# Optimization experiments

Hardware: AMD Instinct MI355X
Metric: run time of the kernel (lower is better)

Reference implementation:

```python
import jax, jax.numpy as jnp
import numpy as np

B, N, E, H = 2, 4096, 512, 8
D = E // H  # head size


def setup_inputs() -> dict:
    key = jax.random.key(0)
    ks = jax.random.split(key, 11)
    s = 1.0 / np.sqrt(E)
    inp = {
        'q': jax.random.normal(ks[0], (B, N, E), jnp.float32),
        'k': jax.random.normal(ks[1], (B, N, E), jnp.float32),
        'v': jax.random.normal(ks[2], (B, N, E), jnp.float32),
        'Wq': jax.random.uniform(ks[3], (E, E), jnp.float32, -s, s),
        'bq': jax.random.uniform(ks[4], (E,), jnp.float32, -s, s),
        'Wk': jax.random.uniform(ks[5], (E, E), jnp.float32, -s, s),
        'bk': jax.random.uniform(ks[6], (E,), jnp.float32, -s, s),
        'Wv': jax.random.uniform(ks[7], (E, E), jnp.float32, -s, s),
        'bv': jax.random.uniform(ks[8], (E,), jnp.float32, -s, s),
        'Wo': jax.random.uniform(ks[9], (E, E), jnp.float32, -s, s),
        'bo': jax.random.uniform(ks[10], (E,), jnp.float32, -s, s),
    }
    return inp


def reference(q, k, v, Wq, bq, Wk, bk, Wv, bv, Wo, bo):
    # Linear projections (torch Linear: x @ W.T + b)
    qp = (q @ Wq.T + bq).reshape(B, N, H, D).transpose(0, 2, 1, 3)  # [B,H,N,D]
    kp = (k @ Wk.T + bk).reshape(B, N, H, D).transpose(0, 2, 1, 3)
    vp = (v @ Wv.T + bv).reshape(B, N, H, D).transpose(0, 2, 1, 3)
    scores = jnp.einsum('bhnd,bhmd->bhnm', qp, kp) / jnp.sqrt(jnp.float32(D))
    attn = jax.nn.softmax(scores, axis=-1)
    out = jnp.einsum('bhnm,bhmd->bhnd', attn, vp)  # [B,H,N,D]
    out = out.transpose(0, 2, 1, 3).reshape(B, N, E)
    return out @ Wo.T + bo
```

## Files before the change

### kernel.cpp

```cpp
#include <hip/hip_runtime.h>
#include <hip/hip_bf16.h>
#include <cstddef>
#include <cstdint>


typedef __bf16 bf16_t;
typedef __bf16 bf16x8 __attribute__((ext_vector_type(8)));
typedef __bf16 bf16x4 __attribute__((ext_vector_type(4)));
typedef float  f32x4  __attribute__((ext_vector_type(4)));

#define MFMA_BF16 __builtin_amdgcn_mfma_f32_16x16x32_bf16

static __device__ __forceinline__ bf16x8 cvt2(const float4& a, const float4& b) {
  return bf16x8{(bf16_t)a.x,(bf16_t)a.y,(bf16_t)a.z,(bf16_t)a.w,
                (bf16_t)b.x,(bf16_t)b.y,(bf16_t)b.z,(bf16_t)b.w};
}

static __device__ __forceinline__ uint32_t pk2(float a, float b) {
  uint32_t r;
  asm("v_cvt_pk_bf16_f32 %0, %1, %2" : "=v"(r) : "v"(a), "v"(b));
  return r;
}

__global__ void __launch_bounds__(256)
cvt_bf16(const float* __restrict__ q, const float* __restrict__ k,
         const float* __restrict__ v, const float* __restrict__ Wq,
         const float* __restrict__ Wk, const float* __restrict__ Wv,
         const float* __restrict__ Wo,
         bf16_t* __restrict__ qb, bf16_t* __restrict__ kb,
         bf16_t* __restrict__ vb, bf16_t* __restrict__ wq,
         bf16_t* __restrict__ wk, bf16_t* __restrict__ wv,
         bf16_t* __restrict__ wo)
{
  const int CQ = 524288;
  const int CW = 32768;
  const int TOT = 3 * CQ + 4 * CW;
  const int STRIDE = 2048 * 256;
  for (int c = blockIdx.x * 256 + threadIdx.x; c < TOT; c += STRIDE) {
    const float* src; bf16_t* dst; int off;
    if (c < 3 * CQ) {
      const int t = c >> 19;
      const int r = c & (CQ - 1);
      src = (t == 0) ? q : (t == 1) ? k : v;
      dst = (t == 0) ? qb : (t == 1) ? kb : vb;
      off = r << 3;
    } else {
      const int c2 = c - 3 * CQ;
      const int t = c2 >> 15;
      const int r = c2 & (CW - 1);
      src = (t == 0) ? Wq : (t == 1) ? Wk : (t == 2) ? Wv : Wo;
      dst = (t == 0) ? wq : (t == 1) ? wk : (t == 2) ? wv : wo;
      off = r << 3;
    }
    const float4 a = *(const float4*)(src + off);
    const float4 b = *(const float4*)(src + off + 4);
    *(bf16x8*)(dst + off) = cvt2(a, b);
  }
}

__global__ void __launch_bounds__(256, 3)
qkv_proj(const bf16_t* __restrict__ qb, const bf16_t* __restrict__ kb,
         const bf16_t* __restrict__ vb,
         const bf16_t* __restrict__ Wqb, const float* __restrict__ bq,
         const bf16_t* __restrict__ Wkb, const float* __restrict__ bk,
         const bf16_t* __restrict__ Wvb, const float* __restrict__ bv,
         bf16_t* __restrict__ Qp, bf16_t* __restrict__ Kp,
         bf16_t* __restrict__ Vt, float qscale)
{
  __shared__ __align__(16) bf16_t S[2 * 128 * 72];
  bf16_t* As = S;
  bf16_t* Bs = S + 128 * 72;

  const int l     = blockIdx.x;
  const int slice = l >> 8;
  const int inner = l & 255;
  const int mtile = ((inner & 7) << 3) | (inner >> 5);
  const int ntile = (inner >> 3) & 3;
  const int tid   = threadIdx.x;
  const int w     = tid >> 6;
  const int lane  = tid & 63;
  const int lr    = lane & 15;
  const int quad  = lane >> 4;
  const int wm    = w & 1;
  const int wn    = w >> 1;
  const int xrow  = tid >> 1, xcol = (tid & 1) << 5;

  const bf16_t* Xb   = (slice == 0) ? qb  : (slice == 1) ? kb  : vb;
  const bf16_t* W    = (slice == 0) ? Wqb : (slice == 1) ? Wkb : Wvb;
  const float*  bias = (slice == 0) ? bq  : (slice == 1) ? bk  : bv;
  const float scale  = (slice == 0) ? qscale : 1.0f;

  float bvv[4];
#pragma unroll
  for (int ci = 0; ci < 4; ++ci) bvv[ci] = bias[ntile * 128 + wn * 64 + ci * 16 + lr];

  f32x4 acc[4][4] = {};
  bf16x8 xa[4], wa[4];

#pragma unroll
  for (int j = 0; j < 4; ++j) {
    xa[j] = *(const bf16x8*)(Xb + (size_t)(mtile * 128 + xrow) * 512 + xcol + j * 8);
    wa[j] = *(const bf16x8*)(W  + (size_t)(ntile * 128 + xrow) * 512 + xcol + j * 8);
  }
#pragma unroll
  for (int j = 0; j < 4; ++j) {
    *(bf16x8*)(&As[xrow * 72 + xcol + j * 8]) = xa[j];
    *(bf16x8*)(&Bs[xrow * 72 + xcol + j * 8]) = wa[j];
  }
  __syncthreads();

  for (int it = 0; it < 8; ++it) {
    if (it != 7) {
      const int k0 = (it + 1) << 6;
#pragma unroll
      for (int j = 0; j < 4; ++j) {
        xa[j] = *(const bf16x8*)(Xb + (size_t)(mtile * 128 + xrow) * 512 + k0 + xcol + j * 8);
        wa[j] = *(const bf16x8*)(W  + (size_t)(ntile * 128 + xrow) * 512 + k0 + xcol + j * 8);
      }
    }
    bf16x8 af[4][2], bfr[4][2];
#pragma unroll
    for (int mi = 0; mi < 4; ++mi)
#pragma unroll
      for (int kh = 0; kh < 2; ++kh)
        af[mi][kh] = *(const bf16x8*)(&As[(wm * 64 + mi * 16 + lr) * 72 + (kh * 4 + quad) * 8]);
#pragma unroll
    for (int ci = 0; ci < 4; ++ci)
#pragma unroll
      for (int kh = 0; kh < 2; ++kh)
        bfr[ci][kh] = *(const bf16x8*)(&Bs[(wn * 64 + ci * 16 + lr) * 72 + (kh * 4 + quad) * 8]);
#pragma unroll
    for (int mi = 0; mi < 4; ++mi)
#pragma unroll
      for (int ci = 0; ci < 4; ++ci) {
        acc[mi][ci] = MFMA_BF16(af[mi][0], bfr[ci][0], acc[mi][ci], 0, 0, 0);
        acc[mi][ci] = MFMA_BF16(af[mi][1], bfr[ci][1], acc[mi][ci], 0, 0, 0);
      }
    __syncthreads();
    if (it != 7) {
#pragma unroll
      for (int j = 0; j < 4; ++j) {
        *(bf16x8*)(&As[xrow * 72 + xcol + j * 8]) = xa[j];
        *(bf16x8*)(&Bs[xrow * 72 + xcol + j * 8]) = wa[j];
      }
      __syncthreads();
    }
  }

  bf16_t (*Ct)[136] = (bf16_t (*)[136])S;
  if (slice < 2) {
    bf16_t* outQK = (slice == 0) ? Qp : Kp;
#pragma unroll
    for (int mi = 0; mi < 4; ++mi)
#pragma unroll
      for (int ci = 0; ci < 4; ++ci)
#pragma unroll
        for (int r = 0; r < 4; ++r)
          Ct[wm * 64 + mi * 16 + quad * 4 + r][wn * 64 + ci * 16 + lr] =
              (bf16_t)((acc[mi][ci][r] + bvv[ci]) * scale);
    __syncthreads();
    const int r2 = tid >> 1, half = tid & 1;
    const int gm = mtile * 128 + r2;
    const int b = gm >> 12, n = gm & 4095;
    const int gc0 = ntile * 128 + half * 64;
    const int h = gc0 >> 6;
    bf16_t* dst = outQK + (size_t)((b * 8 + h) * 4096 + n) * 64;
#pragma unroll
    for (int j = 0; j < 8; ++j)
      *(bf16x8*)(dst + j * 8) = *(const bf16x8*)(&Ct[r2][half * 64 + j * 8]);
  } else {
#pragma unroll
    for (int mi = 0; mi < 4; ++mi)
#pragma unroll
      for (int ci = 0; ci < 4; ++ci)
#pragma unroll
        for (int r = 0; r < 4; ++r)
          Ct[wn * 64 + ci * 16 + lr][wm * 64 + mi * 16 + quad * 4 + r] =
              (bf16_t)(acc[mi][ci][r] + bvv[ci]);
    __syncthreads();
    const int dline = tid >> 1, half = tid & 1;
    const int gc = ntile * 128 + dline;
    const int h = gc >> 6, dd = gc & 63;
    const int b = (mtile * 128) >> 12;
    const int n0 = (mtile * 128) & 4095;
    bf16_t* dst = Vt + (size_t)((b * 8 + h) * 64 + dd) * 4096 + n0 + half * 64;
#pragma unroll
    for (int j = 0; j < 8; ++j)
      *(bf16x8*)(dst + j * 8) = *(const bf16x8*)(&Ct[dline][half * 64 + j * 8]);
  }
}

__global__ void __launch_bounds__(256, 4)
o_proj(const bf16_t* __restrict__ Xb, const bf16_t* __restrict__ W,
       const float* __restrict__ bias, float* __restrict__ out)
{
  __shared__ __align__(16) bf16_t As[64 * 72];
  __shared__ __align__(16) bf16_t Bs[64 * 72];
  const int l     = blockIdx.x;
  const int mtile = ((l & 7) << 4) | ((l >> 3) & 15);
  const int ntile = l >> 7;
  const int tid   = threadIdx.x;
  const int w     = tid >> 6;
  const int lane  = tid & 63;
  const int lr    = lane & 15;
  const int quad  = lane >> 4;
  const int wm    = w & 1;
  const int wn    = w >> 1;
  const int xrow  = tid >> 2, xcol = (tid & 3) << 4;

  float bvv[2];
#pragma unroll
  for (int ci = 0; ci < 2; ++ci) bvv[ci] = bias[ntile * 64 + wn * 32 + ci * 16 + lr];

  f32x4 acc[2][2] = {};
  bf16x8 xb[2], wb[2];

#pragma unroll
  for (int j = 0; j < 2; ++j) {
    xb[j] = *(const bf16x8*)(Xb + (size_t)(mtile * 64 + xrow) * 512 + xcol + j * 8);
    wb[j] = *(const bf16x8*)(W  + (size_t)(ntile * 64 + xrow) * 512 + xcol + j * 8);
  }
#pragma unroll
  for (int j = 0; j < 2; ++j) {
    *(bf16x8*)(&As[xrow * 72 + xcol + j * 8]) = xb[j];
    *(bf16x8*)(&Bs[xrow * 72 + xcol + j * 8]) = wb[j];
  }
  __syncthreads();

  for (int it = 0; it < 8; ++it) {
    if (it != 7) {
      const int k0 = (it + 1) << 6;
#pragma unroll
      for (int j = 0; j < 2; ++j) {
        xb[j] = *(const bf16x8*)(Xb + (size_t)(mtile * 64 + xrow) * 512 + k0 + xcol + j * 8);
        wb[j] = *(const bf16x8*)(W  + (size_t)(ntile * 64 + xrow) * 512 + k0 + xcol + j * 8);
      }
    }
    bf16x8 af[2][2], bfr[2][2];
#pragma unroll
    for (int mi = 0; mi < 2; ++mi)
#pragma unroll
      for (int kh = 0; kh < 2; ++kh)
        af[mi][kh] = *(const bf16x8*)(&As[(wm * 32 + mi * 16 + lr) * 72 + (kh * 4 + quad) * 8]);
#pragma unroll
    for (int ci = 0; ci < 2; ++ci)
#pragma unroll
      for (int kh = 0; kh < 2; ++kh)
        bfr[ci][kh] = *(const bf16x8*)(&Bs[(wn * 32 + ci * 16 + lr) * 72 + (kh * 4 + quad) * 8]);
#pragma unroll
    for (int mi = 0; mi < 2; ++mi)
#pragma unroll
      for (int ci = 0; ci < 2; ++ci) {
        acc[mi][ci] = MFMA_BF16(af[mi][0], bfr[ci][0], acc[mi][ci], 0, 0, 0);
        acc[mi][ci] = MFMA_BF16(af[mi][1], bfr[ci][1], acc[mi][ci], 0, 0, 0);
      }
    __syncthreads();
    if (it != 7) {
#pragma unroll
      for (int j = 0; j < 2; ++j) {
        *(bf16x8*)(&As[xrow * 72 + xcol + j * 8]) = xb[j];
        *(bf16x8*)(&Bs[xrow * 72 + xcol + j * 8]) = wb[j];
      }
      __syncthreads();
    }
  }

#pragma unroll
  for (int mi = 0; mi < 2; ++mi) {
    const int gm0 = mtile * 64 + wm * 32 + mi * 16 + quad * 4;
#pragma unroll
    for (int ci = 0; ci < 2; ++ci) {
      const int gc = ntile * 64 + wn * 32 + ci * 16 + lr;
#pragma unroll
      for (int r = 0; r < 4; ++r)
        out[(size_t)(gm0 + r) * 512 + gc] = acc[mi][ci][r] + bvv[ci];
    }
  }
}

__global__ void __launch_bounds__(512, 2)
flash_attn(const bf16_t* __restrict__ Qp, const bf16_t* __restrict__ Kp,
           const bf16_t* __restrict__ Vt, bf16_t* __restrict__ Oc)
{
  __shared__ __align__(16) bf16_t Klds[2][2][64 * 72];
  __shared__ __align__(16) bf16_t Vlds[2][2][64 * 72];

  const int tid  = threadIdx.x;
  const int w    = tid >> 6;
  const int g    = w >> 2;
  const int wl   = w & 3;
  const int lane = tid & 63, lr = lane & 15, quad = lane >> 4;
  const int bh   = blockIdx.x;
  const int qt0  = blockIdx.y * 128 + wl * 32;

  const bf16_t* Qh = Qp + (size_t)bh * 4096 * 64;
  const bf16_t* Kh = Kp + (size_t)bh * 4096 * 64;
  const bf16_t* Vh = Vt + (size_t)bh * 64 * 4096;

  const int tg   = tid & 255;
  const int srow = tg >> 2;
  const int scol = (tg & 3) << 4;
  const int kvbase = g << 11;

  bf16x8 qf[2][2];
#pragma unroll
  for (int qi = 0; qi < 2; ++qi)
#pragma unroll
    for (int kh = 0; kh < 2; ++kh)
      qf[qi][kh] = *(const bf16x8*)(Qh + (size_t)(qt0 + qi * 16 + lr) * 64 + kh * 32 + quad * 8);

  bf16x8 kst[2], vst[2];
#pragma unroll
  for (int j = 0; j < 2; ++j) {
    kst[j] = *(const bf16x8*)(Kh + (size_t)(kvbase + srow) * 64 + scol + j * 8);
    vst[j] = *(const bf16x8*)(Vh + (size_t)srow * 4096 + kvbase + scol + j * 8);
  }
#pragma unroll
  for (int j = 0; j < 2; ++j) {
    *(bf16x8*)(&Klds[g][0][srow * 72 + scol + j * 8]) = kst[j];
    *(bf16x8*)(&Vlds[g][0][srow * 72 + scol + j * 8]) = vst[j];
  }
  __syncthreads();

  f32x4 acc[2][4] = {};
  float lsum[2] = {0.f, 0.f};
  const f32x4 zero = {0.f, 0.f, 0.f, 0.f};

  for (int it = 0; it < 32; ++it) {
    const int cur = it & 1, nxt = cur ^ 1;

    if (it != 31) {
      const int kvn = kvbase + ((it + 1) << 6);
#pragma unroll
      for (int j = 0; j < 2; ++j) {
        kst[j] = *(const bf16x8*)(Kh + (size_t)(kvn + srow) * 64 + scol + j * 8);
        vst[j] = *(const bf16x8*)(Vh + (size_t)srow * 4096 + kvn + scol + j * 8);
      }
    }

    bf16x8 kf[4][2];
#pragma unroll
    for (int mt = 0; mt < 4; ++mt)
#pragma unroll
      for (int kh = 0; kh < 2; ++kh)
        kf[mt][kh] = *(const bf16x8*)(&Klds[g][cur][(mt * 16 + lr) * 72 + (kh * 4 + quad) * 8]);
    bf16x8 vf[4][2];
#pragma unroll
    for (int t = 0; t < 4; ++t)
#pragma unroll
      for (int kvh = 0; kvh < 2; ++kvh)
        vf[t][kvh] = *(const bf16x8*)(&Vlds[g][cur][(t * 16 + lr) * 72 + (kvh * 4 + quad) * 8]);

    f32x4 sT[4][2];
#pragma unroll
    for (int mt = 0; mt < 4; ++mt)
#pragma unroll
      for (int qi = 0; qi < 2; ++qi) {
        sT[mt][qi] = MFMA_BF16(kf[mt][0], qf[qi][0], zero, 0, 0, 0);
        sT[mt][qi] = MFMA_BF16(kf[mt][1], qf[qi][1], sT[mt][qi], 0, 0, 0);
      }

    bf16x8 pa[2][2];
#pragma unroll
    for (int qi = 0; qi < 2; ++qi) {
      uint32_t ap[4], bp[4];
#pragma unroll
      for (int mt = 0; mt < 4; ++mt) {
        float p0 = __builtin_amdgcn_exp2f(sT[mt][qi][0]);
        float p1 = __builtin_amdgcn_exp2f(sT[mt][qi][1]);
        float p2 = __builtin_amdgcn_exp2f(sT[mt][qi][2]);
        float p3 = __builtin_amdgcn_exp2f(sT[mt][qi][3]);
        lsum[qi] += (p0 + p1) + (p2 + p3);
        ap[mt] = pk2(p0, p1);
        bp[mt] = pk2(p2, p3);
      }
#pragma unroll
      for (int kvh = 0; kvh < 2; ++kvh) {
        uint32_t xa_ = ap[2 * kvh], ya_ = ap[2 * kvh + 1];
        asm("v_permlane32_swap_b32 %0, %1" : "+v"(xa_), "+v"(ya_));
        asm("v_permlane16_swap_b32 %0, %1" : "+v"(xa_), "+v"(ya_));
        uint32_t xb_ = bp[2 * kvh], yb_ = bp[2 * kvh + 1];
        asm("v_permlane32_swap_b32 %0, %1" : "+v"(xb_), "+v"(yb_));
        asm("v_permlane16_swap_b32 %0, %1" : "+v"(xb_), "+v"(yb_));
        union { uint32_t u[4]; bf16x8 v; } pu;
        pu.u[0] = xa_; pu.u[1] = xb_; pu.u[2] = ya_; pu.u[3] = yb_;
        pa[qi][kvh] = pu.v;
      }
    }

#pragma unroll
    for (int t = 0; t < 4; ++t)
#pragma unroll
      for (int qi = 0; qi < 2; ++qi) {
        acc[qi][t] = MFMA_BF16(pa[qi][0], vf[t][0], acc[qi][t], 0, 0, 0);
        acc[qi][t] = MFMA_BF16(pa[qi][1], vf[t][1], acc[qi][t], 0, 0, 0);
      }

    if (it != 31) {
#pragma unroll
      for (int j = 0; j < 2; ++j) {
        *(bf16x8*)(&Klds[g][nxt][srow * 72 + scol + j * 8]) = kst[j];
        *(bf16x8*)(&Vlds[g][nxt][srow * 72 + scol + j * 8]) = vst[j];
      }
    }
    __syncthreads();
  }

#pragma unroll
  for (int qi = 0; qi < 2; ++qi) {
    lsum[qi] += __shfl_xor(lsum[qi], 16);
    lsum[qi] += __shfl_xor(lsum[qi], 32);
  }

  float* accM  = (float*)&Klds[0][0][0];
  float* lsumM = accM + 4 * 64 * 32;
  const int mslot = (wl * 64 + lane);
  if (g == 1) {
#pragma unroll
    for (int qi = 0; qi < 2; ++qi) {
      lsumM[mslot * 2 + qi] = lsum[qi];
#pragma unroll
      for (int t = 0; t < 4; ++t)
#pragma unroll
        for (int r = 0; r < 4; ++r)
          accM[mslot * 32 + qi * 16 + t * 4 + r] = acc[qi][t][r];
    }
  }
  __syncthreads();
  if (g == 1) return;

#pragma unroll
  for (int qi = 0; qi < 2; ++qi) {
    lsum[qi] += lsumM[mslot * 2 + qi];
#pragma unroll
    for (int t = 0; t < 4; ++t)
#pragma unroll
      for (int r = 0; r < 4; ++r)
        acc[qi][t][r] += accM[mslot * 32 + qi * 16 + t * 4 + r];
  }

  const int b = bh >> 3, h = bh & 7;
  bf16_t* Ob = Oc + (size_t)b * 4096 * 512 + h * 64;
#pragma unroll
  for (int qi = 0; qi < 2; ++qi) {
    float inv[4];
#pragma unroll
    for (int r = 0; r < 4; ++r)
      inv[r] = 1.0f / __shfl(lsum[qi], quad * 4 + r);
#pragma unroll
    for (int t = 0; t < 4; ++t)
#pragma unroll
      for (int r = 0; r < 4; ++r) {
        const int n = qt0 + qi * 16 + quad * 4 + r;
        Ob[(size_t)n * 512 + t * 16 + lr] = (bf16_t)(acc[qi][t][r] * inv[r]);
      }
  }
}

extern "C" void kernel_launch(void* const* d_in, const int* in_sizes, int n_in,
                              void* d_out, int out_size, void* d_ws, size_t ws_size,
                              hipStream_t stream)
{
  const float* q  = (const float*)d_in[0];
  const float* k  = (const float*)d_in[1];
  const float* v  = (const float*)d_in[2];
  const float* Wq = (const float*)d_in[3];
  const float* bq = (const float*)d_in[4];
  const float* Wk = (const float*)d_in[5];
  const float* bk = (const float*)d_in[6];
  const float* Wv = (const float*)d_in[7];
  const float* bv = (const float*)d_in[8];
  const float* Wo = (const float*)d_in[9];
  const float* bo = (const float*)d_in[10];

  const size_t HEAD_ELEMS = (size_t)2 * 8 * 4096 * 64;
  const size_t W_ELEMS    = (size_t)512 * 512;

  bf16_t* base = (bf16_t*)d_ws;
  bf16_t* qb  = base;
  bf16_t* kb  = qb + HEAD_ELEMS;
  bf16_t* vb  = kb + HEAD_ELEMS;
  bf16_t* Qp  = vb + HEAD_ELEMS;
  bf16_t* Kp  = Qp + HEAD_ELEMS;
  bf16_t* Vt  = Kp + HEAD_ELEMS;
  bf16_t* wqb = Vt + HEAD_ELEMS;
  bf16_t* wkb = wqb + W_ELEMS;
  bf16_t* wvb = wkb + W_ELEMS;
  bf16_t* wob = wvb + W_ELEMS;
  bf16_t* Oc  = qb;

  const float qscale = 0.125f * 1.44269504f;

  cvt_bf16<<<dim3(2048), 256, 0, stream>>>(q, k, v, Wq, Wk, Wv, Wo,
                                           qb, kb, vb, wqb, wkb, wvb, wob);
  qkv_proj<<<dim3(768), 256, 0, stream>>>(qb, kb, vb, wqb, bq, wkb, bk,
                                          wvb, bv, Qp, Kp, Vt, qscale);
  flash_attn<<<dim3(16, 32), 512, 0, stream>>>(Qp, Kp, Vt, Oc);
  o_proj<<<dim3(1024), 256, 0, stream>>>(Oc, wob, bo, (float*)d_out);
}
```

Measured before the change: 219.7 us.

## Load V fragments directly from global into registers, bypassing LDS

V tiles are no longer staged through shared memory. Each wave loads its own V MFMA fragments straight from global memory into a double-buffered register set (vfA/vfB), prefetching the next chunk while computing the current one. The loop is manually unrolled by two so the register buffers alternate. This removes the V LDS stores and reads and halves the shared-memory footprint, in exchange for higher VGPR pressure and redundant global V reads across the four waves of each group.

```diff
diff --git a/kernel.cpp b/kernel.cpp
--- a/kernel.cpp
+++ b/kernel.cpp
@@ -278,12 +278,84 @@
   }
 }
 
+
+#define FLASH_PHASE(KB, VCUR, VNXT, NXTC)                                      \
+  do {                                                                         \
+    const int nc_ = (NXTC);                                                    \
+    if (nc_ < 32) {                                                            \
+      const int kvn_ = kvbase + (nc_ << 6);                                    \
+      _Pragma("unroll")                                                        \
+      for (int j = 0; j < 2; ++j)                                              \
+        kst[j] = *(const bf16x8*)(Kh + (size_t)(kvn_ + srow) * 64 + scol + j * 8); \
+      _Pragma("unroll")                                                        \
+      for (int t = 0; t < 4; ++t)                                              \
+        _Pragma("unroll")                                                      \
+        for (int kvh = 0; kvh < 2; ++kvh)                                      \
+          VNXT[t][kvh] = *(const bf16x8*)(Vh + (size_t)(t * 16 + lr) * 4096 +  \
+                                          kvn_ + (kvh * 4 + quad) * 8);        \
+    }                                                                          \
+    bf16x8 kf[4][2];                                                           \
+    _Pragma("unroll")                                                          \
+    for (int mt = 0; mt < 4; ++mt)                                             \
+      _Pragma("unroll")                                                        \
+      for (int kh = 0; kh < 2; ++kh)                                           \
+        kf[mt][kh] = *(const bf16x8*)(&Klds[g][KB][(mt * 16 + lr) * 72 +       \
+                                                   (kh * 4 + quad) * 8]);      \
+    f32x4 sT[4][2];                                                            \
+    _Pragma("unroll")                                                          \
+    for (int mt = 0; mt < 4; ++mt)                                             \
+      _Pragma("unroll")                                                        \
+      for (int qi = 0; qi < 2; ++qi) {                                         \
+        sT[mt][qi] = MFMA_BF16(kf[mt][0], qf[qi][0], zero, 0, 0, 0);           \
+        sT[mt][qi] = MFMA_BF16(kf[mt][1], qf[qi][1], sT[mt][qi], 0, 0, 0);     \
+      }                                                                        \
+    bf16x8 pa[2][2];                                                           \
+    _Pragma("unroll")                                                          \
+    for (int qi = 0; qi < 2; ++qi) {                                           \
+      uint32_t ap[4], bp[4];                                                   \
+      _Pragma("unroll")                                                        \
+      for (int mt = 0; mt < 4; ++mt) {                                         \
+        float p0 = __builtin_amdgcn_exp2f(sT[mt][qi][0]);                      \
+        float p1 = __builtin_amdgcn_exp2f(sT[mt][qi][1]);                      \
+        float p2 = __builtin_amdgcn_exp2f(sT[mt][qi][2]);                      \
+        float p3 = __builtin_amdgcn_exp2f(sT[mt][qi][3]);                      \
+        lsum[qi] += (p0 + p1) + (p2 + p3);                                     \
+        ap[mt] = pk2(p0, p1);                                                  \
+        bp[mt] = pk2(p2, p3);                                                  \
+      }                                                                        \
+      _Pragma("unroll")                                                        \
+      for (int kvh = 0; kvh < 2; ++kvh) {                                      \
+        uint32_t xa_ = ap[2 * kvh], ya_ = ap[2 * kvh + 1];                     \
+        asm("v_permlane32_swap_b32 %0, %1" : "+v"(xa_), "+v"(ya_));            \
+        asm("v_permlane16_swap_b32 %0, %1" : "+v"(xa_), "+v"(ya_));            \
+        uint32_t xb_ = bp[2 * kvh], yb_ = bp[2 * kvh + 1];                     \
+        asm("v_permlane32_swap_b32 %0, %1" : "+v"(xb_), "+v"(yb_));            \
+        asm("v_permlane16_swap_b32 %0, %1" : "+v"(xb_), "+v"(yb_));            \
+        union { uint32_t u[4]; bf16x8 v; } pu;                                 \
+        pu.u[0] = xa_; pu.u[1] = xb_; pu.u[2] = ya_; pu.u[3] = yb_;            \
+        pa[qi][kvh] = pu.v;                                                    \
+      }                                                                        \
+    }                                                                          \
+    _Pragma("unroll")                                                          \
+    for (int t = 0; t < 4; ++t)                                                \
+      _Pragma("unroll")                                                        \
+      for (int qi = 0; qi < 2; ++qi) {                                         \
+        acc[qi][t] = MFMA_BF16(pa[qi][0], VCUR[t][0], acc[qi][t], 0, 0, 0);    \
+        acc[qi][t] = MFMA_BF16(pa[qi][1], VCUR[t][1], acc[qi][t], 0, 0, 0);    \
+      }                                                                        \
+    if (nc_ < 32) {                                                            \
+      _Pragma("unroll")                                                        \
+      for (int j = 0; j < 2; ++j)                                              \
+        *(bf16x8*)(&Klds[g][KB ^ 1][srow * 72 + scol + j * 8]) = kst[j];       \
+    }                                                                          \
+    __syncthreads();                                                           \
+  } while (0)
+
 __global__ void __launch_bounds__(512, 2)
 flash_attn(const bf16_t* __restrict__ Qp, const bf16_t* __restrict__ Kp,
            const bf16_t* __restrict__ Vt, bf16_t* __restrict__ Oc)
 {
   __shared__ __align__(16) bf16_t Klds[2][2][64 * 72];
-  __shared__ __align__(16) bf16_t Vlds[2][2][64 * 72];
 
   const int tid  = threadIdx.x;
   const int w    = tid >> 6;
@@ -309,101 +381,29 @@
     for (int kh = 0; kh < 2; ++kh)
       qf[qi][kh] = *(const bf16x8*)(Qh + (size_t)(qt0 + qi * 16 + lr) * 64 + kh * 32 + quad * 8);
 
-  bf16x8 kst[2], vst[2];
-#pragma unroll
-  for (int j = 0; j < 2; ++j) {
+  bf16x8 kst[2];
+  bf16x8 vfA[4][2], vfB[4][2];
+#pragma unroll
+  for (int j = 0; j < 2; ++j)
     kst[j] = *(const bf16x8*)(Kh + (size_t)(kvbase + srow) * 64 + scol + j * 8);
-    vst[j] = *(const bf16x8*)(Vh + (size_t)srow * 4096 + kvbase + scol + j * 8);
-  }
-#pragma unroll
-  for (int j = 0; j < 2; ++j) {
+#pragma unroll
+  for (int t = 0; t < 4; ++t)
+#pragma unroll
+    for (int kvh = 0; kvh < 2; ++kvh)
+      vfA[t][kvh] = *(const bf16x8*)(Vh + (size_t)(t * 16 + lr) * 4096 +
+                                     kvbase + (kvh * 4 + quad) * 8);
+#pragma unroll
+  for (int j = 0; j < 2; ++j)
     *(bf16x8*)(&Klds[g][0][srow * 72 + scol + j * 8]) = kst[j];
-    *(bf16x8*)(&Vlds[g][0][srow * 72 + scol + j * 8]) = vst[j];
-  }
   __syncthreads();
 
   f32x4 acc[2][4] = {};
   float lsum[2] = {0.f, 0.f};
   const f32x4 zero = {0.f, 0.f, 0.f, 0.f};
 
-  for (int it = 0; it < 32; ++it) {
-    const int cur = it & 1, nxt = cur ^ 1;
-
-    if (it != 31) {
-      const int kvn = kvbase + ((it + 1) << 6);
-#pragma unroll
-      for (int j = 0; j < 2; ++j) {
-        kst[j] = *(const bf16x8*)(Kh + (size_t)(kvn + srow) * 64 + scol + j * 8);
-        vst[j] = *(const bf16x8*)(Vh + (size_t)srow * 4096 + kvn + scol + j * 8);
-      }
-    }
-
-    bf16x8 kf[4][2];
-#pragma unroll
-    for (int mt = 0; mt < 4; ++mt)
-#pragma unroll
-      for (int kh = 0; kh < 2; ++kh)
-        kf[mt][kh] = *(const bf16x8*)(&Klds[g][cur][(mt * 16 + lr) * 72 + (kh * 4 + quad) * 8]);
-    bf16x8 vf[4][2];
-#pragma unroll
-    for (int t = 0; t < 4; ++t)
-#pragma unroll
-      for (int kvh = 0; kvh < 2; ++kvh)
-        vf[t][kvh] = *(const bf16x8*)(&Vlds[g][cur][(t * 16 + lr) * 72 + (kvh * 4 + quad) * 8]);
-
-    f32x4 sT[4][2];
-#pragma unroll
-    for (int mt = 0; mt < 4; ++mt)
-#pragma unroll
-      for (int qi = 0; qi < 2; ++qi) {
-        sT[mt][qi] = MFMA_BF16(kf[mt][0], qf[qi][0], zero, 0, 0, 0);
-        sT[mt][qi] = MFMA_BF16(kf[mt][1], qf[qi][1], sT[mt][qi], 0, 0, 0);
-      }
-
-    bf16x8 pa[2][2];
-#pragma unroll
-    for (int qi = 0; qi < 2; ++qi) {
-      uint32_t ap[4], bp[4];
-#pragma unroll
-      for (int mt = 0; mt < 4; ++mt) {
-        float p0 = __builtin_amdgcn_exp2f(sT[mt][qi][0]);
-        float p1 = __builtin_amdgcn_exp2f(sT[mt][qi][1]);
-        float p2 = __builtin_amdgcn_exp2f(sT[mt][qi][2]);
-        float p3 = __builtin_amdgcn_exp2f(sT[mt][qi][3]);
-        lsum[qi] += (p0 + p1) + (p2 + p3);
-        ap[mt] = pk2(p0, p1);
-        bp[mt] = pk2(p2, p3);
-      }
-#pragma unroll
-      for (int kvh = 0; kvh < 2; ++kvh) {
-        uint32_t xa_ = ap[2 * kvh], ya_ = ap[2 * kvh + 1];
-        asm("v_permlane32_swap_b32 %0, %1" : "+v"(xa_), "+v"(ya_));
-        asm("v_permlane16_swap_b32 %0, %1" : "+v"(xa_), "+v"(ya_));
-        uint32_t xb_ = bp[2 * kvh], yb_ = bp[2 * kvh + 1];
-        asm("v_permlane32_swap_b32 %0, %1" : "+v"(xb_), "+v"(yb_));
-        asm("v_permlane16_swap_b32 %0, %1" : "+v"(xb_), "+v"(yb_));
-        union { uint32_t u[4]; bf16x8 v; } pu;
-        pu.u[0] = xa_; pu.u[1] = xb_; pu.u[2] = ya_; pu.u[3] = yb_;
-        pa[qi][kvh] = pu.v;
-      }
-    }
-
-#pragma unroll
-    for (int t = 0; t < 4; ++t)
-#pragma unroll
-      for (int qi = 0; qi < 2; ++qi) {
-        acc[qi][t] = MFMA_BF16(pa[qi][0], vf[t][0], acc[qi][t], 0, 0, 0);
-        acc[qi][t] = MFMA_BF16(pa[qi][1], vf[t][1], acc[qi][t], 0, 0, 0);
-      }
-
-    if (it != 31) {
-#pragma unroll
-      for (int j = 0; j < 2; ++j) {
-        *(bf16x8*)(&Klds[g][nxt][srow * 72 + scol + j * 8]) = kst[j];
-        *(bf16x8*)(&Vlds[g][nxt][srow * 72 + scol + j * 8]) = vst[j];
-      }
-    }
-    __syncthreads();
+  for (int c = 0; c < 32; c += 2) {
+    FLASH_PHASE(0, vfA, vfB, c + 1);
+    FLASH_PHASE(1, vfB, vfA, c + 2);
   }
 
 #pragma unroll
```

Result: slower. 298.7 us (+35.9%).
